# Optimization experiments

Hardware: AMD Instinct MI355X
Metric: run time of the kernel (lower is better)

Reference implementation:

```python
import jax, jax.numpy as jnp
import numpy as np

B, T, X, H, Z, G, Y = 4096, 32, 256, 256, 256, 128, 2


def _xavier(key, fan_in, fan_out):
    lim = float(np.sqrt(6.0 / (fan_in + fan_out)))
    return jax.random.uniform(key, (fan_in, fan_out), jnp.float32, -lim, lim)


def setup_inputs() -> dict:
    key = jax.random.key(0)
    ks = jax.random.split(key, 18)
    return {
        "x": jax.random.normal(ks[0], (B, T, X), jnp.float32),
        "y_ph": jax.random.uniform(ks[1], (B, T, Y), jnp.float32),
        "T_ph": jax.random.randint(ks[2], (B,), 1, T + 1),  # 1..T valid days
        "h0": jnp.tanh(jax.random.normal(ks[3], (B, H), jnp.float32)),   # tanh(randn) init state
        "z0": jnp.tanh(jax.random.normal(ks[4], (B, Z), jnp.float32)),
        "eps": jax.random.normal(ks[5], (T, B, Z), jnp.float32),          # reparam noise per step
        # gate / candidate nets: fan_in = x + h + z
        "Wr": _xavier(ks[6], X + H + Z, H), "br": jnp.zeros((H,), jnp.float32),
        "Wu": _xavier(ks[7], X + H + Z, H), "bu": jnp.zeros((H,), jnp.float32),
        "Wh": _xavier(ks[8], X + H + Z, H), "bh": jnp.zeros((H,), jnp.float32),
        # prior latent net: fan_in = x + h
        "Wzp": _xavier(ks[9], X + H, Z), "bzp": jnp.zeros((Z,), jnp.float32),
        "Wpm": _xavier(ks[10], Z, Z), "bpm": jnp.zeros((Z,), jnp.float32),
        "Wps": _xavier(ks[11], Z, Z), "bps": jnp.zeros((Z,), jnp.float32),
        # posterior latent net: fan_in = x + h + y
        "Wzq": _xavier(ks[12], X + H + Y, Z), "bzq": jnp.zeros((Z,), jnp.float32),
        "Wqm": _xavier(ks[13], Z, Z), "bqm": jnp.zeros((Z,), jnp.float32),
        "Wqs": _xavier(ks[14], Z, Z), "bqs": jnp.zeros((Z,), jnp.float32),
        # output nets
        "Wg": _xavier(ks[15], X + H + Z, G), "bg": jnp.zeros((G,), jnp.float32),
        "Wy": _xavier(ks[16], G, Y), "by": jnp.zeros((Y,), jnp.float32),
    }


def reference(x, y_ph, T_ph, h0, z0, eps,
              Wr, br, Wu, bu, Wh, bh,
              Wzp, bzp, Wpm, bpm, Wps, bps,
              Wzq, bzq, Wqm, bqm, Wqs, bqs,
              Wg, bg, Wy, by):
    x_t = jnp.transpose(x, (1, 0, 2))     # [T, B, X]
    y_t = jnp.transpose(y_ph, (1, 0, 2))  # [T, B, Y]

    def step(carry, inp):
        h_prev, z_prev = carry
        xt, yt, et = inp
        ga = jnp.concatenate([xt, h_prev, z_prev], axis=-1)
        r = jax.nn.sigmoid(ga @ Wr + br)
        u = jax.nn.sigmoid(ga @ Wu + bu)
        ha = jnp.concatenate([xt, r * h_prev, z_prev], axis=-1)
        h_tilde = jnp.tanh(ha @ Wh + bh)
        h = (1.0 - u) * h_prev + u * h_tilde
        # prior p(z_t | x_t, h_t): z_prior = mean (is_prior=True)
        hzp = jnp.tanh(jnp.concatenate([xt, h], axis=-1) @ Wzp + bzp)
        mu_p = hzp @ Wpm + bpm
        sd_p = jnp.sqrt(jnp.exp(hzp @ Wps + bps))
        z_prior = mu_p
        # posterior q(z_t | x_t, h_t, y_t): reparameterized sample
        hzq = jnp.tanh(jnp.concatenate([xt, h, yt], axis=-1) @ Wzq + bzq)
        mu_q = hzq @ Wqm + bqm
        sd_q = jnp.sqrt(jnp.exp(hzq @ Wqs + bqs))
        z_post = mu_q + sd_q * et
        # KL(q || p) for diagonal Normals
        kl = jnp.log(sd_p / sd_q) + (sd_q ** 2 + (mu_q - mu_p) ** 2) / (2.0 * sd_p ** 2) - 0.5
        return (h, z_post), (h, z_post, z_prior, kl)

    (_, _), (h_s, z_post, z_prior, kl) = jax.lax.scan(step, (h0, z0), (x_t, y_t, eps))
    h_s = jnp.transpose(h_s, (1, 0, 2))      # [B, T, H]
    z_post = jnp.transpose(z_post, (1, 0, 2))
    kl = jnp.transpose(kl, (1, 0, 2)).sum(axis=-1)  # [B, T]

    g = jnp.tanh(jnp.concatenate([x, h_s, z_post], axis=-1) @ Wg + bg)  # [B, T, G]
    y = jax.nn.softmax(g @ Wy + by, axis=-1)                             # [B, T, Y]
    g_T = g[jnp.arange(x.shape[0]), T_ph - 1]                            # [B, G] (training, daily_att)
    return (y, kl, g_T)
```

## Files before the change

### kernel.cpp

```cpp
#include <hip/hip_runtime.h>

typedef unsigned short u16;
typedef unsigned int u32;
typedef __attribute__((ext_vector_type(8))) short short8;
typedef __attribute__((ext_vector_type(4))) float float4v;

#define B_SZ 4096
#define T_SZ 32
#define XD 256
#define HD 256
#define ZD 256
#define GD 128
#define YD 2

#define BM 32
#define NW 16

#define W1_OFF 0
#define W2_OFF 393216
#define W3_OFF 589824
#define W4_OFF 868352
#define WG_OFF 1130496
#define WTOT   1228800

#define YTOT  (B_SZ*T_SZ*YD)
#define KLTOT (B_SZ*T_SZ)

#define HST 260
#define UST 264

__device__ __forceinline__ u16 f2bf(float f) {
    u32 u = __float_as_uint(f);
    u32 r = (u + 0x7fffu + ((u >> 16) & 1u)) >> 16;
    return (u16)r;
}
__device__ __forceinline__ float bf2f(u16 h) {
    return __uint_as_float(((u32)h) << 16);
}
__device__ __forceinline__ float tanh_f(float x) {
    float e = __expf(2.f * x);
    return 1.f - 2.f / (e + 1.f);
}
__device__ __forceinline__ float sigm_f(float x) {
    return 1.f / (1.f + __expf(-x));
}

__device__ __forceinline__ int aga_off(int r, int k) {
    return (((r >> 4) * 24 + (k >> 5)) << 9) + ((((k >> 3) & 3) * 16 + (r & 15)) << 3) + (k & 7);
}
__device__ __forceinline__ int a3s_off(int r, int k, int pq) {
    return (((pq * 2 + (r >> 4)) * 8 + (k >> 5)) << 9) + ((((k >> 3) & 3) * 16 + (r & 15)) << 3) + (k & 7);
}

#define MFMA(a, b, c) __builtin_amdgcn_mfma_f32_16x16x32_bf16(a, b, c, 0, 0, 0)

__global__ void prep_weights(const float* __restrict__ Wr, const float* __restrict__ Wu,
                             const float* __restrict__ Wh, const float* __restrict__ Wzp,
                             const float* __restrict__ Wzq, const float* __restrict__ Wpm,
                             const float* __restrict__ Wps, const float* __restrict__ Wqm,
                             const float* __restrict__ Wqs, const float* __restrict__ Wg,
                             u16* __restrict__ wts)
{
    int o = blockIdx.x * 256 + threadIdx.x;
    if (o >= WTOT) return;
    int mat, w, KT;
    if (o < W2_OFF)      { mat = 0; w = o;          KT = 24; }
    else if (o < W3_OFF) { mat = 1; w = o - W2_OFF; KT = 24; }
    else if (o < W4_OFF) { mat = 2; w = o - W3_OFF; KT = 17; }
    else if (o < WG_OFF) { mat = 3; w = o - W4_OFF; KT = 8;  }
    else                 { mat = 4; w = o - WG_OFF; KT = 24; }
    int nt  = w / (KT * 512);
    int rem = w - nt * (KT * 512);
    int kt  = rem >> 9;
    int q   = rem & 511;
    int lane = q >> 3, j = q & 7;
    int n = (nt << 4) | (lane & 15);
    int k = (kt << 5) + ((lane >> 4) << 3) + j;
    float v = 0.f;
    switch (mat) {
        case 0: v = (n < 256) ? Wr[k * 256 + n] : Wu[k * 256 + (n - 256)]; break;
        case 1: v = Wh[k * 256 + n]; break;
        case 2: v = (n < 256) ? (k < 512 ? Wzp[k * 256 + n] : 0.f)
                              : (k < 514 ? Wzq[k * 256 + (n - 256)] : 0.f); break;
        case 3: { int sel = n >> 8; int nn = n & 255;
                  const float* s = (sel == 0) ? Wpm : (sel == 1) ? Wps : (sel == 2) ? Wqm : Wqs;
                  v = s[k * 256 + nn]; } break;
        default: v = Wg[k * 128 + n]; break;
    }
    wts[o] = f2bf(v);
}

__global__ __launch_bounds__(1024, 4) void vrnn_all(
    const float* __restrict__ x,   const float* __restrict__ y_ph,
    const int*   __restrict__ Tph, const float* __restrict__ h0,
    const float* __restrict__ z0,  const float* __restrict__ eps,
    const float* __restrict__ br,  const float* __restrict__ bu,
    const float* __restrict__ bh,  const float* __restrict__ bzp,
    const float* __restrict__ bpm, const float* __restrict__ bps,
    const float* __restrict__ bzq, const float* __restrict__ bqm,
    const float* __restrict__ bqs, const float* __restrict__ bg,
    const float* __restrict__ by,  const float* __restrict__ Wy,
    const u16*   __restrict__ wts, float* __restrict__ out)
{
    __shared__ __align__(16) u16   a_ga[48 * 512];
    __shared__ __align__(16) u16   a3s[32 * 512];
    __shared__ __align__(16) float h32[BM * HST];
    __shared__ __align__(16) u16   u_bf[BM * UST];
    __shared__ float part[8 * BM * 2];
    __shared__ float kl_acc[BM];
    __shared__ int   tph_s[BM];

    const int tid  = threadIdx.x;
    const int wv   = tid >> 6;
    const int lane = tid & 63;
    const int quad = lane >> 4;
    const int l15  = lane & 15;
    const int b0   = blockIdx.x * BM;

    const int c10 = wv * 32 + l15;
    const float bs1_0 = (c10 < 256) ? br[c10] : bu[c10 - 256];
    const float bs1_1 = (c10 + 16 < 256) ? br[c10 + 16] : bu[c10 + 16 - 256];
    const int c2  = wv * 16 + l15;
    const float bh_r = bh[c2];
    const float bz0 = (c10 < 256) ? bzp[c10] : bzq[c10 - 256];
    const float bz1 = (c10 + 16 < 256) ? bzp[c10 + 16] : bzq[c10 + 16 - 256];
    const int zc  = wv * 16 + l15;
    const float b4pm = bpm[zc], b4ps = bps[zc], b4qm = bqm[zc], b4qs = bqs[zc];
    const int c5  = (wv >> 1) * 16 + l15;
    const int mt5 = wv & 1;
    const float bg_r = bg[c5];
    const float wy0 = Wy[c5 * 2], wy1 = Wy[c5 * 2 + 1];
    const float by0 = by[0], by1 = by[1];

    if (tid < BM) tph_s[tid] = Tph[b0 + tid];

    {
        int r = tid >> 5, cc = (tid & 31) * 8;
        const float* hp = &h0[(b0 + r) * HD + cc];
        const float* zp = &z0[(b0 + r) * ZD + cc];
        short8 hv, zv;
#pragma unroll
        for (int j = 0; j < 8; ++j) {
            float hh = hp[j];
            h32[r * HST + cc + j] = hh;
            hv[j] = (short)f2bf(hh);
            zv[j] = (short)f2bf(zp[j]);
        }
        *(short8*)&a_ga[aga_off(r, 256 + cc)] = hv;
        *(short8*)&a_ga[aga_off(r, 512 + cc)] = zv;
    }
    __syncthreads();

    const float4v zero4 = {0.f, 0.f, 0.f, 0.f};

    for (int t = 0; t < T_SZ; ++t) {
        {
            int r = tid >> 5, cc = (tid & 31) * 8;
            const float* xp = &x[((size_t)(b0 + r) * T_SZ + t) * XD + cc];
            short8 xv;
#pragma unroll
            for (int j = 0; j < 8; ++j) xv[j] = (short)f2bf(xp[j]);
            *(short8*)&a_ga[aga_off(r, cc)] = xv;
        }
        __syncthreads();

        {
            const u16* pB0 = wts + W1_OFF + (((wv * 2    ) * 24) << 9) + lane * 8;
            const u16* pB1 = wts + W1_OFF + (((wv * 2 + 1) * 24) << 9) + lane * 8;
            float4v a00 = zero4, a01 = zero4, a10 = zero4, a11 = zero4;
            short8 b0c = *(const short8*)pB0;
            short8 b1c = *(const short8*)pB1;
            for (int kt = 0; kt < 24; ++kt) {
                int kn = (kt < 23) ? kt + 1 : 23;
                short8 b0n = *(const short8*)(pB0 + (kn << 9));
                short8 b1n = *(const short8*)(pB1 + (kn << 9));
                short8 aF0 = *(const short8*)&a_ga[(kt << 9) + lane * 8];
                short8 aF1 = *(const short8*)&a_ga[((24 + kt) << 9) + lane * 8];
                a00 = MFMA(aF0, b0c, a00); a01 = MFMA(aF0, b1c, a01);
                a10 = MFMA(aF1, b0c, a10); a11 = MFMA(aF1, b1c, a11);
                b0c = b0n; b1c = b1n;
            }
            __syncthreads();
#pragma unroll
            for (int mt = 0; mt < 2; ++mt) {
                const float4v* am = (mt == 0) ? &a00 : &a10;
                const float4v* an = (mt == 0) ? &a01 : &a11;
#pragma unroll
                for (int i = 0; i < 4; ++i) {
                    int row = mt * 16 + quad * 4 + i;
                    {
                        int c = c10;
                        float v = (*am)[i];
                        if (c < 256) {
                            float rr = sigm_f(v + bs1_0);
                            a_ga[aga_off(row, 256 + c)] = f2bf(rr * h32[row * HST + c]);
                        } else {
                            u_bf[row * UST + (c - 256)] = f2bf(sigm_f(v + bs1_0));
                        }
                    }
                    {
                        int c = c10 + 16;
                        float v = (*an)[i];
                        if (c < 256) {
                            float rr = sigm_f(v + bs1_1);
                            a_ga[aga_off(row, 256 + c)] = f2bf(rr * h32[row * HST + c]);
                        } else {
                            u_bf[row * UST + (c - 256)] = f2bf(sigm_f(v + bs1_1));
                        }
                    }
                }
            }
            __syncthreads();
        }

        {
            const u16* pB = wts + W2_OFF + ((wv * 24) << 9) + lane * 8;
            float4v a0 = zero4, a1 = zero4;
            short8 bc = *(const short8*)pB;
            for (int kt = 0; kt < 24; ++kt) {
                int kn = (kt < 23) ? kt + 1 : 23;
                short8 bn = *(const short8*)(pB + (kn << 9));
                short8 aF0 = *(const short8*)&a_ga[(kt << 9) + lane * 8];
                short8 aF1 = *(const short8*)&a_ga[((24 + kt) << 9) + lane * 8];
                a0 = MFMA(aF0, bc, a0);
                a1 = MFMA(aF1, bc, a1);
                bc = bn;
            }
            __syncthreads();
#pragma unroll
            for (int mt = 0; mt < 2; ++mt) {
                const float4v* am = (mt == 0) ? &a0 : &a1;
#pragma unroll
                for (int i = 0; i < 4; ++i) {
                    int row = mt * 16 + quad * 4 + i;
                    float ht = tanh_f((*am)[i] + bh_r);
                    float uu = bf2f(u_bf[row * UST + c2]);
                    float hp = h32[row * HST + c2];
                    float h  = (1.f - uu) * hp + uu * ht;
                    h32[row * HST + c2] = h;
                    a_ga[aga_off(row, 256 + c2)] = f2bf(h);
                }
            }
            if (tid < 128) {
                int r = tid >> 2, grp = tid & 3;
                short8 v = {0, 0, 0, 0, 0, 0, 0, 0};
                if (grp == 0) {
                    const float* yp = &y_ph[((size_t)(b0 + r) * T_SZ + t) * YD];
                    v[0] = (short)f2bf(yp[0]);
                    v[1] = (short)f2bf(yp[1]);
                }
                *(short8*)&a_ga[aga_off(r, 512 + grp * 8)] = v;
            }
            __syncthreads();
        }

        {
            const u16* pB0 = wts + W3_OFF + (((wv * 2    ) * 17) << 9) + lane * 8;
            const u16* pB1 = wts + W3_OFF + (((wv * 2 + 1) * 17) << 9) + lane * 8;
            float4v a00 = zero4, a01 = zero4, a10 = zero4, a11 = zero4;
            short8 b0c = *(const short8*)pB0;
            short8 b1c = *(const short8*)pB1;
            for (int kt = 0; kt < 17; ++kt) {
                int kn = (kt < 16) ? kt + 1 : 16;
                short8 b0n = *(const short8*)(pB0 + (kn << 9));
                short8 b1n = *(const short8*)(pB1 + (kn << 9));
                short8 aF0 = *(const short8*)&a_ga[(kt << 9) + lane * 8];
                short8 aF1 = *(const short8*)&a_ga[((24 + kt) << 9) + lane * 8];
                a00 = MFMA(aF0, b0c, a00); a01 = MFMA(aF0, b1c, a01);
                a10 = MFMA(aF1, b0c, a10); a11 = MFMA(aF1, b1c, a11);
                b0c = b0n; b1c = b1n;
            }
#pragma unroll
            for (int mt = 0; mt < 2; ++mt) {
                const float4v* am = (mt == 0) ? &a00 : &a10;
                const float4v* an = (mt == 0) ? &a01 : &a11;
#pragma unroll
                for (int i = 0; i < 4; ++i) {
                    int row = mt * 16 + quad * 4 + i;
                    {
                        int c = c10;
                        float hz = tanh_f((*am)[i] + bz0);
                        a3s[a3s_off(row, c & 255, c >> 8)] = f2bf(hz);
                    }
                    {
                        int c = c10 + 16;
                        float hz = tanh_f((*an)[i] + bz1);
                        a3s[a3s_off(row, c & 255, c >> 8)] = f2bf(hz);
                    }
                }
            }
            if (tid < BM) kl_acc[tid] = 0.f;
            __syncthreads();
        }

        {
            const u16* pB0 = wts + W4_OFF + (((0 * 16 + wv) * 8) << 9) + lane * 8;
            const u16* pB1 = wts + W4_OFF + (((1 * 16 + wv) * 8) << 9) + lane * 8;
            const u16* pB2 = wts + W4_OFF + (((2 * 16 + wv) * 8) << 9) + lane * 8;
            const u16* pB3 = wts + W4_OFF + (((3 * 16 + wv) * 8) << 9) + lane * 8;
            float4v ac[4][2];
#pragma unroll
            for (int m = 0; m < 4; ++m) { ac[m][0] = zero4; ac[m][1] = zero4; }
            for (int kt = 0; kt < 8; ++kt) {
                short8 bm0 = *(const short8*)(pB0 + (kt << 9));
                short8 bm1 = *(const short8*)(pB1 + (kt << 9));
                short8 bm2 = *(const short8*)(pB2 + (kt << 9));
                short8 bm3 = *(const short8*)(pB3 + (kt << 9));
                short8 aP0 = *(const short8*)&a3s[((0 + kt) << 9) + lane * 8];
                short8 aP1 = *(const short8*)&a3s[((8 + kt) << 9) + lane * 8];
                short8 aQ0 = *(const short8*)&a3s[((16 + kt) << 9) + lane * 8];
                short8 aQ1 = *(const short8*)&a3s[((24 + kt) << 9) + lane * 8];
                ac[0][0] = MFMA(aP0, bm0, ac[0][0]); ac[0][1] = MFMA(aP1, bm0, ac[0][1]);
                ac[1][0] = MFMA(aP0, bm1, ac[1][0]); ac[1][1] = MFMA(aP1, bm1, ac[1][1]);
                ac[2][0] = MFMA(aQ0, bm2, ac[2][0]); ac[2][1] = MFMA(aQ1, bm2, ac[2][1]);
                ac[3][0] = MFMA(aQ0, bm3, ac[3][0]); ac[3][1] = MFMA(aQ1, bm3, ac[3][1]);
            }
            float kls[2][4];
#pragma unroll
            for (int mt = 0; mt < 2; ++mt)
#pragma unroll
                for (int i = 0; i < 4; ++i) {
                    int row = mt * 16 + quad * 4 + i;
                    float mu_p = ac[0][mt][i] + b4pm;
                    float s_p  = ac[1][mt][i] + b4ps;
                    float mu_q = ac[2][mt][i] + b4qm;
                    float s_q  = ac[3][mt][i] + b4qs;
                    float e = eps[((size_t)t * B_SZ + (b0 + row)) * ZD + zc];
                    float zpost = mu_q + __expf(0.5f * s_q) * e;
                    float dmu = mu_q - mu_p;
                    kls[mt][i] = 0.5f * (s_p - s_q)
                               + (__expf(s_q) + dmu * dmu) * 0.5f * __expf(-s_p) - 0.5f;
                    a_ga[aga_off(row, 512 + zc)] = f2bf(zpost);
                }
#pragma unroll
            for (int mt = 0; mt < 2; ++mt)
#pragma unroll
                for (int i = 0; i < 4; ++i) {
                    float v = kls[mt][i];
                    v += __shfl_xor(v, 1); v += __shfl_xor(v, 2);
                    v += __shfl_xor(v, 4); v += __shfl_xor(v, 8);
                    if (l15 == 0) atomicAdd(&kl_acc[mt * 16 + quad * 4 + i], v);
                }
            __syncthreads();
            if (tid < BM)
                out[YTOT + (size_t)(b0 + tid) * T_SZ + t] = kl_acc[tid];
        }

        {
            const u16* pB = wts + WG_OFF + (((wv >> 1) * 24) << 9) + lane * 8;
            float4v a5 = zero4;
            short8 bc = *(const short8*)pB;
            const int abase = mt5 * 24;
            for (int kt = 0; kt < 24; ++kt) {
                int kn = (kt < 23) ? kt + 1 : 23;
                short8 bn = *(const short8*)(pB + (kn << 9));
                short8 aF = *(const short8*)&a_ga[((abase + kt) << 9) + lane * 8];
                a5 = MFMA(aF, bc, a5);
                bc = bn;
            }
            float g[4];
#pragma unroll
            for (int i = 0; i < 4; ++i) {
                int row = mt5 * 16 + quad * 4 + i;
                g[i] = tanh_f(a5[i] + bg_r);
                if (tph_s[row] - 1 == t)
                    out[YTOT + KLTOT + (size_t)(b0 + row) * GD + c5] = g[i];
            }
#pragma unroll
            for (int i = 0; i < 4; ++i) {
                float p0 = g[i] * wy0, p1 = g[i] * wy1;
                p0 += __shfl_xor(p0, 1); p0 += __shfl_xor(p0, 2);
                p0 += __shfl_xor(p0, 4); p0 += __shfl_xor(p0, 8);
                p1 += __shfl_xor(p1, 1); p1 += __shfl_xor(p1, 2);
                p1 += __shfl_xor(p1, 4); p1 += __shfl_xor(p1, 8);
                if (l15 == 0) {
                    int row = mt5 * 16 + quad * 4 + i;
                    part[((wv >> 1) * BM + row) * 2]     = p0;
                    part[((wv >> 1) * BM + row) * 2 + 1] = p1;
                }
            }
            __syncthreads();
            if (tid < BM) {
                int r = tid;
                float s0 = by0, s1 = by1;
#pragma unroll
                for (int j = 0; j < 8; ++j) {
                    s0 += part[(j * BM + r) * 2];
                    s1 += part[(j * BM + r) * 2 + 1];
                }
                float mx = fmaxf(s0, s1);
                float e0 = __expf(s0 - mx), e1 = __expf(s1 - mx);
                float inv = 1.f / (e0 + e1);
                size_t yoff = ((size_t)(b0 + r) * T_SZ + t) * YD;
                out[yoff]     = e0 * inv;
                out[yoff + 1] = e1 * inv;
            }
        }
    }
}

extern "C" void kernel_launch(void* const* d_in, const int* in_sizes, int n_in,
                              void* d_out, int out_size, void* d_ws, size_t ws_size,
                              hipStream_t stream)
{
    const float* x   = (const float*)d_in[0];
    const float* yph = (const float*)d_in[1];
    const int*   Tph = (const int*)  d_in[2];
    const float* h0  = (const float*)d_in[3];
    const float* z0  = (const float*)d_in[4];
    const float* eps = (const float*)d_in[5];
    const float* Wr  = (const float*)d_in[6];
    const float* br  = (const float*)d_in[7];
    const float* Wu  = (const float*)d_in[8];
    const float* bu  = (const float*)d_in[9];
    const float* Wh  = (const float*)d_in[10];
    const float* bh  = (const float*)d_in[11];
    const float* Wzp = (const float*)d_in[12];
    const float* bzp = (const float*)d_in[13];
    const float* Wpm = (const float*)d_in[14];
    const float* bpm = (const float*)d_in[15];
    const float* Wps = (const float*)d_in[16];
    const float* bps = (const float*)d_in[17];
    const float* Wzq = (const float*)d_in[18];
    const float* bzq = (const float*)d_in[19];
    const float* Wqm = (const float*)d_in[20];
    const float* bqm = (const float*)d_in[21];
    const float* Wqs = (const float*)d_in[22];
    const float* bqs = (const float*)d_in[23];
    const float* Wg  = (const float*)d_in[24];
    const float* bg  = (const float*)d_in[25];
    const float* Wy  = (const float*)d_in[26];
    const float* by  = (const float*)d_in[27];
    u16*   wts = (u16*)d_ws;
    float* out = (float*)d_out;

    hipLaunchKernelGGL(prep_weights, dim3((WTOT + 255) / 256), dim3(256), 0, stream,
                       Wr, Wu, Wh, Wzp, Wzq, Wpm, Wps, Wqm, Wqs, Wg, wts);
    hipLaunchKernelGGL(vrnn_all, dim3(B_SZ / BM), dim3(1024), 0, stream,
                       x, yph, Tph, h0, z0, eps, br, bu, bh, bzp, bpm, bps,
                       bzq, bqm, bqs, bg, by, Wy, wts, out);
}
```

Baseline: 4.714 ms.

## Deepen weight prefetch, prefetch next-step x and eps, use nontemporal memory ops

Each GEMM loop is fully unrolled and keeps a four-deep (two-deep for the latent heads) register ring of weight fragments instead of one-ahead prefetch. The next timestep's x slice is loaded during the output GEMM of the current step, and the eps values are loaded before the posterior GEMM, so global latency overlaps compute. Streaming inputs and outputs use nontemporal loads and stores to avoid polluting cache. The extra live registers may lower occupancy or cause spills.

```diff
diff --git a/kernel.cpp b/kernel.cpp
--- a/kernel.cpp
+++ b/kernel.cpp
@@ -134,20 +134,35 @@
 
     if (tid < BM) tph_s[tid] = Tph[b0 + tid];
 
+    const int xr  = tid >> 5;
+    const int xcc = (tid & 31) * 8;
+
+    float4v xn0, xn1;
     {
-        int r = tid >> 5, cc = (tid & 31) * 8;
-        const float* hp = &h0[(b0 + r) * HD + cc];
-        const float* zp = &z0[(b0 + r) * ZD + cc];
+        const float* xp = &x[((size_t)(b0 + xr) * T_SZ + 0) * XD + xcc];
+        xn0 = __builtin_nontemporal_load((const float4v*)xp);
+        xn1 = __builtin_nontemporal_load((const float4v*)(xp + 4));
+    }
+
+    {
+        const float* hp = &h0[(b0 + xr) * HD + xcc];
+        const float* zp = &z0[(b0 + xr) * ZD + xcc];
+        float4v ha = __builtin_nontemporal_load((const float4v*)hp);
+        float4v hb = __builtin_nontemporal_load((const float4v*)(hp + 4));
+        float4v za = __builtin_nontemporal_load((const float4v*)zp);
+        float4v zb = __builtin_nontemporal_load((const float4v*)(zp + 4));
         short8 hv, zv;
 #pragma unroll
-        for (int j = 0; j < 8; ++j) {
-            float hh = hp[j];
-            h32[r * HST + cc + j] = hh;
-            hv[j] = (short)f2bf(hh);
-            zv[j] = (short)f2bf(zp[j]);
-        }
-        *(short8*)&a_ga[aga_off(r, 256 + cc)] = hv;
-        *(short8*)&a_ga[aga_off(r, 512 + cc)] = zv;
+        for (int j = 0; j < 4; ++j) {
+            h32[xr * HST + xcc + j]     = ha[j];
+            h32[xr * HST + xcc + 4 + j] = hb[j];
+            hv[j]     = (short)f2bf(ha[j]);
+            hv[4 + j] = (short)f2bf(hb[j]);
+            zv[j]     = (short)f2bf(za[j]);
+            zv[4 + j] = (short)f2bf(zb[j]);
+        }
+        *(short8*)&a_ga[aga_off(xr, 256 + xcc)] = hv;
+        *(short8*)&a_ga[aga_off(xr, 512 + xcc)] = zv;
     }
     __syncthreads();
 
@@ -155,30 +170,38 @@
 
     for (int t = 0; t < T_SZ; ++t) {
         {
-            int r = tid >> 5, cc = (tid & 31) * 8;
-            const float* xp = &x[((size_t)(b0 + r) * T_SZ + t) * XD + cc];
             short8 xv;
 #pragma unroll
-            for (int j = 0; j < 8; ++j) xv[j] = (short)f2bf(xp[j]);
-            *(short8*)&a_ga[aga_off(r, cc)] = xv;
+            for (int j = 0; j < 4; ++j) {
+                xv[j]     = (short)f2bf(xn0[j]);
+                xv[4 + j] = (short)f2bf(xn1[j]);
+            }
+            *(short8*)&a_ga[aga_off(xr, xcc)] = xv;
         }
         __syncthreads();
 
         {
             const u16* pB0 = wts + W1_OFF + (((wv * 2    ) * 24) << 9) + lane * 8;
             const u16* pB1 = wts + W1_OFF + (((wv * 2 + 1) * 24) << 9) + lane * 8;
+            short8 b0r[4], b1r[4];
+#pragma unroll
+            for (int p = 0; p < 4; ++p) {
+                b0r[p] = *(const short8*)(pB0 + (p << 9));
+                b1r[p] = *(const short8*)(pB1 + (p << 9));
+            }
             float4v a00 = zero4, a01 = zero4, a10 = zero4, a11 = zero4;
-            short8 b0c = *(const short8*)pB0;
-            short8 b1c = *(const short8*)pB1;
+#pragma unroll
             for (int kt = 0; kt < 24; ++kt) {
-                int kn = (kt < 23) ? kt + 1 : 23;
-                short8 b0n = *(const short8*)(pB0 + (kn << 9));
-                short8 b1n = *(const short8*)(pB1 + (kn << 9));
                 short8 aF0 = *(const short8*)&a_ga[(kt << 9) + lane * 8];
                 short8 aF1 = *(const short8*)&a_ga[((24 + kt) << 9) + lane * 8];
-                a00 = MFMA(aF0, b0c, a00); a01 = MFMA(aF0, b1c, a01);
-                a10 = MFMA(aF1, b0c, a10); a11 = MFMA(aF1, b1c, a11);
-                b0c = b0n; b1c = b1n;
+                short8 bc0 = b0r[kt & 3];
+                short8 bc1 = b1r[kt & 3];
+                if (kt + 4 < 24) {
+                    b0r[kt & 3] = *(const short8*)(pB0 + ((kt + 4) << 9));
+                    b1r[kt & 3] = *(const short8*)(pB1 + ((kt + 4) << 9));
+                }
+                a00 = MFMA(aF0, bc0, a00); a01 = MFMA(aF0, bc1, a01);
+                a10 = MFMA(aF1, bc0, a10); a11 = MFMA(aF1, bc1, a11);
             }
             __syncthreads();
 #pragma unroll
@@ -215,16 +238,20 @@
 
         {
             const u16* pB = wts + W2_OFF + ((wv * 24) << 9) + lane * 8;
+            short8 bcr[4];
+#pragma unroll
+            for (int p = 0; p < 4; ++p)
+                bcr[p] = *(const short8*)(pB + (p << 9));
             float4v a0 = zero4, a1 = zero4;
-            short8 bc = *(const short8*)pB;
+#pragma unroll
             for (int kt = 0; kt < 24; ++kt) {
-                int kn = (kt < 23) ? kt + 1 : 23;
-                short8 bn = *(const short8*)(pB + (kn << 9));
                 short8 aF0 = *(const short8*)&a_ga[(kt << 9) + lane * 8];
                 short8 aF1 = *(const short8*)&a_ga[((24 + kt) << 9) + lane * 8];
+                short8 bc = bcr[kt & 3];
+                if (kt + 4 < 24)
+                    bcr[kt & 3] = *(const short8*)(pB + ((kt + 4) << 9));
                 a0 = MFMA(aF0, bc, a0);
                 a1 = MFMA(aF1, bc, a1);
-                bc = bn;
             }
             __syncthreads();
 #pragma unroll
@@ -246,29 +273,46 @@
                 short8 v = {0, 0, 0, 0, 0, 0, 0, 0};
                 if (grp == 0) {
                     const float* yp = &y_ph[((size_t)(b0 + r) * T_SZ + t) * YD];
-                    v[0] = (short)f2bf(yp[0]);
-                    v[1] = (short)f2bf(yp[1]);
+                    v[0] = (short)f2bf(__builtin_nontemporal_load(yp));
+                    v[1] = (short)f2bf(__builtin_nontemporal_load(yp + 1));
                 }
                 *(short8*)&a_ga[aga_off(r, 512 + grp * 8)] = v;
             }
             __syncthreads();
         }
 
+        float er[2][4];
         {
+#pragma unroll
+            for (int mt = 0; mt < 2; ++mt)
+#pragma unroll
+                for (int i = 0; i < 4; ++i) {
+                    int row = mt * 16 + quad * 4 + i;
+                    er[mt][i] = __builtin_nontemporal_load(
+                        &eps[((size_t)t * B_SZ + (b0 + row)) * ZD + zc]);
+                }
+
             const u16* pB0 = wts + W3_OFF + (((wv * 2    ) * 17) << 9) + lane * 8;
             const u16* pB1 = wts + W3_OFF + (((wv * 2 + 1) * 17) << 9) + lane * 8;
+            short8 b0r[4], b1r[4];
+#pragma unroll
+            for (int p = 0; p < 4; ++p) {
+                b0r[p] = *(const short8*)(pB0 + (p << 9));
+                b1r[p] = *(const short8*)(pB1 + (p << 9));
+            }
             float4v a00 = zero4, a01 = zero4, a10 = zero4, a11 = zero4;
-            short8 b0c = *(const short8*)pB0;
-            short8 b1c = *(const short8*)pB1;
+#pragma unroll
             for (int kt = 0; kt < 17; ++kt) {
-                int kn = (kt < 16) ? kt + 1 : 16;
-                short8 b0n = *(const short8*)(pB0 + (kn << 9));
-                short8 b1n = *(const short8*)(pB1 + (kn << 9));
                 short8 aF0 = *(const short8*)&a_ga[(kt << 9) + lane * 8];
                 short8 aF1 = *(const short8*)&a_ga[((24 + kt) << 9) + lane * 8];
-                a00 = MFMA(aF0, b0c, a00); a01 = MFMA(aF0, b1c, a01);
-                a10 = MFMA(aF1, b0c, a10); a11 = MFMA(aF1, b1c, a11);
-                b0c = b0n; b1c = b1n;
+                short8 bc0 = b0r[kt & 3];
+                short8 bc1 = b1r[kt & 3];
+                if (kt + 4 < 17) {
+                    b0r[kt & 3] = *(const short8*)(pB0 + ((kt + 4) << 9));
+                    b1r[kt & 3] = *(const short8*)(pB1 + ((kt + 4) << 9));
+                }
+                a00 = MFMA(aF0, bc0, a00); a01 = MFMA(aF0, bc1, a01);
+                a10 = MFMA(aF1, bc0, a10); a11 = MFMA(aF1, bc1, a11);
             }
 #pragma unroll
             for (int mt = 0; mt < 2; ++mt) {
@@ -298,14 +342,27 @@
             const u16* pB1 = wts + W4_OFF + (((1 * 16 + wv) * 8) << 9) + lane * 8;
             const u16* pB2 = wts + W4_OFF + (((2 * 16 + wv) * 8) << 9) + lane * 8;
             const u16* pB3 = wts + W4_OFF + (((3 * 16 + wv) * 8) << 9) + lane * 8;
+            short8 r0[2], r1[2], r2[2], r3[2];
+#pragma unroll
+            for (int p = 0; p < 2; ++p) {
+                r0[p] = *(const short8*)(pB0 + (p << 9));
+                r1[p] = *(const short8*)(pB1 + (p << 9));
+                r2[p] = *(const short8*)(pB2 + (p << 9));
+                r3[p] = *(const short8*)(pB3 + (p << 9));
+            }
             float4v ac[4][2];
 #pragma unroll
             for (int m = 0; m < 4; ++m) { ac[m][0] = zero4; ac[m][1] = zero4; }
+#pragma unroll
             for (int kt = 0; kt < 8; ++kt) {
-                short8 bm0 = *(const short8*)(pB0 + (kt << 9));
-                short8 bm1 = *(const short8*)(pB1 + (kt << 9));
-                short8 bm2 = *(const short8*)(pB2 + (kt << 9));
-                short8 bm3 = *(const short8*)(pB3 + (kt << 9));
+                short8 bm0 = r0[kt & 1], bm1 = r1[kt & 1];
+                short8 bm2 = r2[kt & 1], bm3 = r3[kt & 1];
+                if (kt + 2 < 8) {
+                    r0[kt & 1] = *(const short8*)(pB0 + ((kt + 2) << 9));
+                    r1[kt & 1] = *(const short8*)(pB1 + ((kt + 2) << 9));
+                    r2[kt & 1] = *(const short8*)(pB2 + ((kt + 2) << 9));
+                    r3[kt & 1] = *(const short8*)(pB3 + ((kt + 2) << 9));
+                }
                 short8 aP0 = *(const short8*)&a3s[((0 + kt) << 9) + lane * 8];
                 short8 aP1 = *(const short8*)&a3s[((8 + kt) << 9) + lane * 8];
                 short8 aQ0 = *(const short8*)&a3s[((16 + kt) << 9) + lane * 8];
@@ -325,7 +382,7 @@
                     float s_p  = ac[1][mt][i] + b4ps;
                     float mu_q = ac[2][mt][i] + b4qm;
                     float s_q  = ac[3][mt][i] + b4qs;
-                    float e = eps[((size_t)t * B_SZ + (b0 + row)) * ZD + zc];
+                    float e = er[mt][i];
                     float zpost = mu_q + __expf(0.5f * s_q) * e;
                     float dmu = mu_q - mu_p;
                     kls[mt][i] = 0.5f * (s_p - s_q)
@@ -343,20 +400,30 @@
                 }
             __syncthreads();
             if (tid < BM)
-                out[YTOT + (size_t)(b0 + tid) * T_SZ + t] = kl_acc[tid];
+                __builtin_nontemporal_store(kl_acc[tid],
+                    &out[YTOT + (size_t)(b0 + tid) * T_SZ + t]);
         }
 
         {
             const u16* pB = wts + WG_OFF + (((wv >> 1) * 24) << 9) + lane * 8;
+            if (t + 1 < T_SZ) {
+                const float* xp = &x[((size_t)(b0 + xr) * T_SZ + (t + 1)) * XD + xcc];
+                xn0 = __builtin_nontemporal_load((const float4v*)xp);
+                xn1 = __builtin_nontemporal_load((const float4v*)(xp + 4));
+            }
+            short8 wgr[4];
+#pragma unroll
+            for (int p = 0; p < 4; ++p)
+                wgr[p] = *(const short8*)(pB + (p << 9));
             float4v a5 = zero4;
-            short8 bc = *(const short8*)pB;
             const int abase = mt5 * 24;
+#pragma unroll
             for (int kt = 0; kt < 24; ++kt) {
-                int kn = (kt < 23) ? kt + 1 : 23;
-                short8 bn = *(const short8*)(pB + (kn << 9));
                 short8 aF = *(const short8*)&a_ga[((abase + kt) << 9) + lane * 8];
+                short8 bc = wgr[kt & 3];
+                if (kt + 4 < 24)
+                    wgr[kt & 3] = *(const short8*)(pB + ((kt + 4) << 9));
                 a5 = MFMA(aF, bc, a5);
-                bc = bn;
             }
             float g[4];
 #pragma unroll
@@ -364,7 +431,8 @@
                 int row = mt5 * 16 + quad * 4 + i;
                 g[i] = tanh_f(a5[i] + bg_r);
                 if (tph_s[row] - 1 == t)
-                    out[YTOT + KLTOT + (size_t)(b0 + row) * GD + c5] = g[i];
+                    __builtin_nontemporal_store(g[i],
+                        &out[YTOT + KLTOT + (size_t)(b0 + row) * GD + c5]);
             }
 #pragma unroll
             for (int i = 0; i < 4; ++i) {
@@ -392,8 +460,8 @@
                 float e0 = __expf(s0 - mx), e1 = __expf(s1 - mx);
                 float inv = 1.f / (e0 + e1);
                 size_t yoff = ((size_t)(b0 + r) * T_SZ + t) * YD;
-                out[yoff]     = e0 * inv;
-                out[yoff + 1] = e1 * inv;
+                __builtin_nontemporal_store(e0 * inv, &out[yoff]);
+                __builtin_nontemporal_store(e1 * inv, &out[yoff + 1]);
             }
         }
     }
```

New measurement: 4.783 ms. Within noise of the previous version (+1.5%).
